# Kernel optimization log

Measured on AMD Instinct MI355X. Metric: run time of the kernel, lower is better.

## Reference

```python
import jax, jax.numpy as jnp
import numpy as np

NUM_REP = 3

def setup_inputs() -> dict:
    N, E, DIM, R2, L, B, NEG = 20000, 100000, 32, 100, 4, 4, 32
    ks = jax.random.split(jax.random.key(0), 12)
    # all negatives in a row share the same head (required by the model's assert)
    h = jax.random.randint(ks[0], (B, 1), 0, N)
    t = jax.random.randint(ks[1], (B, NEG), 0, N)
    batch = jnp.stack([jnp.broadcast_to(h, (B, NEG)), t], axis=-1)  # [B,NEG,2]
    edge_index = jax.random.randint(ks[2], (2, E), 0, N)
    edge_type = jax.random.randint(ks[3], (E,), 0, R2)
    edge_attr = 0.1 * jax.random.normal(ks[4], (E, DIM), jnp.float32)
    start_query = jax.random.normal(ks[5], (NUM_REP, DIM), jnp.float32)
    W_rel = jax.random.normal(ks[6], (L, DIM, R2 * DIM), jnp.float32) * (DIM ** -0.5)
    b_rel = jnp.zeros((L, R2 * DIM), jnp.float32)
    W_lin = jax.random.normal(ks[7], (L, 2 * DIM, DIM), jnp.float32) * ((2 * DIM) ** -0.5)
    b_lin = jnp.zeros((L, DIM), jnp.float32)
    W_mlp1 = jax.random.normal(ks[8], (DIM, DIM), jnp.float32) * (DIM ** -0.5)
    b_mlp1 = jnp.zeros((DIM,), jnp.float32)
    W_mlp2 = jax.random.normal(ks[9], (DIM, DIM), jnp.float32) * (DIM ** -0.5)
    b_mlp2 = jnp.zeros((DIM,), jnp.float32)
    return {"batch": batch, "edge_index": edge_index, "edge_type": edge_type,
            "edge_attr": edge_attr, "num_nodes": N, "start_query": start_query,
            "W_rel": W_rel, "b_rel": b_rel, "W_lin": W_lin, "b_lin": b_lin,
            "W_mlp1": W_mlp1, "b_mlp1": b_mlp1, "W_mlp2": W_mlp2, "b_mlp2": b_mlp2}

def reference(batch, edge_index, edge_type, edge_attr, num_nodes, start_query,
              W_rel, b_rel, W_lin, b_lin, W_mlp1, b_mlp1, W_mlp2, b_mlp2):
    B, num_neg, _ = batch.shape
    N = int(num_nodes)
    dim = start_query.shape[1]
    L = W_rel.shape[0]
    bs = NUM_REP * B
    batch_full = jnp.tile(batch, (NUM_REP, 1, 1))            # [bs, neg, 2]
    query_idx = jnp.repeat(jnp.arange(NUM_REP), B)           # [bs]
    h_index, t_index = batch_full[..., 0], batch_full[..., 1]
    # negative_sample_to_tail (no-op when heads are constant per row, as built)
    is_t_neg = jnp.all(h_index == h_index[:, :1], axis=-1, keepdims=True)
    h_index, t_index = (jnp.where(is_t_neg, h_index, t_index),
                        jnp.where(is_t_neg, t_index, h_index))
    h0 = h_index[:, 0]
    q = start_query[query_idx]                               # [bs, dim]
    rows = jnp.arange(bs)
    boundary = jnp.zeros((bs, N, dim), q.dtype).at[rows, h0].add(q)
    pb = jnp.zeros((bs, N), q.dtype).at[rows, h0].set(1.0)   # path boundary
    src, dst = edge_index[0], edge_index[1]
    x = boundary
    for l in range(L):
        # dependent per-query relation embeddings: [bs, 2R, dim]
        rel = (q @ W_rel[l] + b_rel[l]).reshape(bs, -1, dim)
        rel_e = rel[:, edge_type] + edge_attr[None]          # [bs, E, dim]
        msg = x[:, src] * rel_e                              # distmult message
        # sum aggregation; boundary acts as the self-loop message
        agg = jnp.zeros((bs, N, dim), x.dtype).at[:, dst].add(msg) + boundary
        x = jax.nn.relu(jnp.concatenate([x, agg], axis=-1) @ W_lin[l] + b_lin[l])
        # reachability propagation of the path boundary (scatter-max)
        pb = jnp.maximum(pb, jnp.zeros((bs, N), pb.dtype).at[:, dst].max(pb[:, src]))
    feat_t = x[rows[:, None], t_index]                       # [bs, neg, dim]
    feat = feat_t.reshape(NUM_REP, B, num_neg, dim).mean(0)  # mean over reps
    features = jax.nn.relu(feat @ W_mlp1 + b_mlp1) @ W_mlp2 + b_mlp2
    pb_t = pb[rows[:, None], t_index][..., None]             # [bs, neg, 1]
    path_boundary = pb_t.reshape(NUM_REP, B, num_neg, 1).max(0)
    return features, path_boundary
```

## Files before the change

### kernel.cpp

```cpp
#include <hip/hip_runtime.h>

#define N_NODES 20000
#define N_EDGES 100000
#define DIM 32
#define R2 100
#define NLAYERS 4
#define BATCH 4
#define NEG 32
#define NREP 3
#define BS (NREP * BATCH)
#define RELDIM (R2 * DIM)

#define NPB 4
#define TPN 96
#define LBLK (NPB * TPN)
#define GRID_LAYER (N_NODES / NPB)

#define XO_A 0
#define XO_B (XO_A + (size_t)N_NODES * BS * DIM)
#define PBO_A (XO_B + (size_t)N_NODES * BS * DIM)
#define PBO_B (PBO_A + (size_t)N_NODES * BS)
#define RELO (PBO_B + (size_t)N_NODES * BS)
#define QO (RELO + (size_t)NLAYERS * R2 * BS * DIM)
#define FLOAT_TOTAL (QO + (size_t)BS * DIM)

#define IO_H0 0
#define IO_TIDX (IO_H0 + BS)
#define IO_COUNTS (IO_TIDX + BS * NEG)
#define IO_OFF (IO_COUNTS + N_NODES)
#define IO_CURSOR (IO_OFF + N_NODES + 1)
#define IO_PERM (IO_CURSOR + N_NODES)
#define INT_TOTAL (IO_PERM + N_EDGES)

__global__ void k_init(const int* __restrict__ batch,
                       const float* __restrict__ start_query,
                       float* __restrict__ q, int* __restrict__ h0,
                       int* __restrict__ t_idx) {
    int r = threadIdx.x;
    if (r >= BS) return;
    int b = r % BATCH, rep = r / BATCH;
    int h00 = batch[(b * NEG + 0) * 2 + 0];
    bool is_t_neg = true;
    for (int j = 0; j < NEG; j++)
        if (batch[(b * NEG + j) * 2 + 0] != h00) { is_t_neg = false; break; }
    int hsel = is_t_neg ? 0 : 1;
    int h0v = batch[(b * NEG + 0) * 2 + hsel];
    h0[r] = h0v;
    for (int j = 0; j < NEG; j++)
        t_idx[r * NEG + j] = batch[(b * NEG + j) * 2 + (1 - hsel)];
    for (int d = 0; d < DIM; d++) q[r * DIM + d] = start_query[rep * DIM + d];
}

__global__ void k_count(const int* __restrict__ dst, int* __restrict__ counts) {
    int e = blockIdx.x * blockDim.x + threadIdx.x;
    if (e < N_EDGES) atomicAdd(&counts[dst[e]], 1);
}

__global__ void k_scan(const int* __restrict__ counts, int* __restrict__ off,
                       int* __restrict__ cursor) {
    __shared__ int sd[1024];
    int t = threadIdx.x;
    const int CH = (N_NODES + 1023) / 1024;
    int base = t * CH;
    int sum = 0;
    for (int i = 0; i < CH; i++) {
        int idx = base + i;
        if (idx < N_NODES) sum += counts[idx];
    }
    sd[t] = sum;
    __syncthreads();
    for (int o = 1; o < 1024; o <<= 1) {
        int v = (t >= o) ? sd[t - o] : 0;
        __syncthreads();
        sd[t] += v;
        __syncthreads();
    }
    int excl = sd[t] - sum;
    int run = excl;
    for (int i = 0; i < CH; i++) {
        int idx = base + i;
        if (idx < N_NODES) {
            off[idx] = run;
            cursor[idx] = run;
            run += counts[idx];
        }
    }
    if (t == 1023) off[N_NODES] = sd[1023];
}

__global__ void k_place(const int* __restrict__ dst, int* __restrict__ cursor,
                        int* __restrict__ perm) {
    int e = blockIdx.x * blockDim.x + threadIdx.x;
    if (e < N_EDGES) {
        int p = atomicAdd(&cursor[dst[e]], 1);
        perm[p] = e;
    }
}

__global__ void k_rel_all(const float* __restrict__ q, const float* __restrict__ W_rel,
                          const float* __restrict__ b_rel, float* __restrict__ rel) {
    int idx = blockIdx.x * blockDim.x + threadIdx.x;
    if (idx >= NLAYERS * R2 * BS * DIM) return;
    int d = idx & 31;
    int r = (idx >> 5) % BS;
    int et = (idx / (BS * DIM)) % R2;
    int l = idx / (R2 * BS * DIM);
    int c = et * DIM + d;
    const float* W = W_rel + (size_t)l * DIM * RELDIM;
    float acc = b_rel[l * RELDIM + c];
    #pragma unroll
    for (int k = 0; k < DIM; k++) acc += q[r * DIM + k] * W[(size_t)k * RELDIM + c];
    rel[idx] = acc;
}

template <bool L0>
__launch_bounds__(LBLK)
__global__ void k_layer(const float* __restrict__ x_old, const float* __restrict__ pb_old,
                        const float* __restrict__ rel_l, const float* __restrict__ edge_attr,
                        const int* __restrict__ src, const int* __restrict__ etype,
                        const int* __restrict__ off, const int* __restrict__ perm,
                        const int* __restrict__ h0, const float* __restrict__ q,
                        const float* __restrict__ W_lin_l, const float* __restrict__ b_lin_l,
                        float* __restrict__ x_new, float* __restrict__ pb_new) {
    __shared__ float sW[64 * DIM];
    __shared__ float sB[DIM];
    __shared__ float sIn[NPB * BS * 68];

    for (int i = threadIdx.x; i < 64 * DIM; i += LBLK) sW[i] = W_lin_l[i];
    if (threadIdx.x < DIM) sB[threadIdx.x] = b_lin_l[threadIdx.x];

    const int gi = threadIdx.x / TPN;
    const int t = threadIdx.x % TPN;
    const int r = t >> 3;
    const int l = t & 7;
    const int n = blockIdx.x * NPB + gi;

    const int h0r = h0[r];
    const float4 q4 = *(const float4*)(q + r * DIM + l * 4);

    float4 xr4, ag4 = make_float4(0.f, 0.f, 0.f, 0.f);
    float pbm;
    if (L0) {
        xr4 = (n == h0r) ? q4 : make_float4(0.f, 0.f, 0.f, 0.f);
        pbm = (n == h0r) ? 1.f : 0.f;
    } else {
        xr4 = *(const float4*)(x_old + ((size_t)n * BS + r) * DIM + l * 4);
        pbm = pb_old[n * BS + r];
    }

    const int s0 = off[n], s1 = off[n + 1];
    for (int k = s0; k < s1; k++) {
        int e = perm[k];
        int s = src[e];
        if (L0) {
            if (s == h0r) {
                int et = etype[e];
                float4 rl = *(const float4*)(rel_l + ((size_t)et * BS + r) * DIM + l * 4);
                float4 ea = *(const float4*)(edge_attr + (size_t)e * DIM + l * 4);
                ag4.x += q4.x * (rl.x + ea.x);
                ag4.y += q4.y * (rl.y + ea.y);
                ag4.z += q4.z * (rl.z + ea.z);
                ag4.w += q4.w * (rl.w + ea.w);
                pbm = 1.f;
            }
        } else {
            int et = etype[e];
            float4 xs = *(const float4*)(x_old + ((size_t)s * BS + r) * DIM + l * 4);
            float4 rl = *(const float4*)(rel_l + ((size_t)et * BS + r) * DIM + l * 4);
            float4 ea = *(const float4*)(edge_attr + (size_t)e * DIM + l * 4);
            ag4.x += xs.x * (rl.x + ea.x);
            ag4.y += xs.y * (rl.y + ea.y);
            ag4.z += xs.z * (rl.z + ea.z);
            ag4.w += xs.w * (rl.w + ea.w);
            pbm = fmaxf(pbm, pb_old[s * BS + r]);
        }
    }
    if (n == h0r) {
        ag4.x += q4.x; ag4.y += q4.y; ag4.z += q4.z; ag4.w += q4.w;
    }

    float* srow = sIn + (gi * BS + r) * 68;
    *(float4*)(srow + l * 4) = xr4;
    *(float4*)(srow + 32 + l * 4) = ag4;
    __syncthreads();

    float4 acc = *(const float4*)(sB + l * 4);
    #pragma unroll
    for (int k4 = 0; k4 < 16; k4++) {
        float4 v = *(const float4*)(srow + k4 * 4);
        const float* wb = sW + (k4 * 4) * DIM + l * 4;
        float4 w0 = *(const float4*)(wb);
        float4 w1 = *(const float4*)(wb + DIM);
        float4 w2 = *(const float4*)(wb + 2 * DIM);
        float4 w3 = *(const float4*)(wb + 3 * DIM);
        acc.x += v.x * w0.x + v.y * w1.x + v.z * w2.x + v.w * w3.x;
        acc.y += v.x * w0.y + v.y * w1.y + v.z * w2.y + v.w * w3.y;
        acc.z += v.x * w0.z + v.y * w1.z + v.z * w2.z + v.w * w3.z;
        acc.w += v.x * w0.w + v.y * w1.w + v.z * w2.w + v.w * w3.w;
    }
    acc.x = fmaxf(acc.x, 0.f);
    acc.y = fmaxf(acc.y, 0.f);
    acc.z = fmaxf(acc.z, 0.f);
    acc.w = fmaxf(acc.w, 0.f);
    *(float4*)(x_new + ((size_t)n * BS + r) * DIM + l * 4) = acc;
    if (l == 0) pb_new[n * BS + r] = pbm;
}

__launch_bounds__(1024)
__global__ void k_final(const float* __restrict__ x, const float* __restrict__ pb,
                        const int* __restrict__ t_idx,
                        const float* __restrict__ W1, const float* __restrict__ b1,
                        const float* __restrict__ W2, const float* __restrict__ b2,
                        float* __restrict__ out) {
    __shared__ float sW1[DIM * DIM];
    __shared__ float sW2[DIM * DIM];
    __shared__ float sfeat[BATCH * NEG * DIM];
    __shared__ float shid[BATCH * NEG * DIM];
    const int t = threadIdx.x;
    const int NPAIR = BATCH * NEG;

    for (int i = t; i < DIM * DIM; i += 1024) { sW1[i] = W1[i]; sW2[i] = W2[i]; }

    for (int i = t; i < NPAIR * DIM; i += 1024) {
        int pair = i >> 5;
        int d = i & 31;
        int b = pair >> 5;
        int tt = t_idx[pair];
        float s = 0.f;
        #pragma unroll
        for (int rep = 0; rep < NREP; rep++)
            s += x[((size_t)tt * BS + rep * BATCH + b) * DIM + d];
        sfeat[i] = s * (1.f / 3.f);
    }
    __syncthreads();

    for (int i = t; i < NPAIR * DIM; i += 1024) {
        int pair = i >> 5;
        int jj = i & 31;
        float a = b1[jj];
        #pragma unroll
        for (int k = 0; k < DIM; k++)
            a += sfeat[pair * DIM + k] * sW1[k * DIM + jj];
        shid[i] = fmaxf(a, 0.f);
    }
    __syncthreads();

    for (int i = t; i < NPAIR * DIM; i += 1024) {
        int pair = i >> 5;
        int jj = i & 31;
        float a = b2[jj];
        #pragma unroll
        for (int k = 0; k < DIM; k++)
            a += shid[pair * DIM + k] * sW2[k * DIM + jj];
        out[i] = a;
    }

    if (t < NPAIR) {
        int b = t >> 5;
        int tt = t_idx[t];
        float pm = 0.f;
        #pragma unroll
        for (int rep = 0; rep < NREP; rep++)
            pm = fmaxf(pm, pb[(size_t)tt * BS + rep * BATCH + b]);
        out[NPAIR * DIM + t] = pm;
    }
}

extern "C" void kernel_launch(void* const* d_in, const int* in_sizes, int n_in,
                              void* d_out, int out_size, void* d_ws, size_t ws_size,
                              hipStream_t stream) {
    const int* batch = (const int*)d_in[0];
    const int* edge_index = (const int*)d_in[1];
    const int* edge_type = (const int*)d_in[2];
    const float* edge_attr = (const float*)d_in[3];
    const float* start_query = (const float*)d_in[5];
    const float* W_rel = (const float*)d_in[6];
    const float* b_rel = (const float*)d_in[7];
    const float* W_lin = (const float*)d_in[8];
    const float* b_lin = (const float*)d_in[9];
    const float* W_mlp1 = (const float*)d_in[10];
    const float* b_mlp1 = (const float*)d_in[11];
    const float* W_mlp2 = (const float*)d_in[12];
    const float* b_mlp2 = (const float*)d_in[13];

    float* wf = (float*)d_ws;
    int* wi = (int*)(wf + FLOAT_TOTAL);
    size_t need = FLOAT_TOTAL * sizeof(float) + INT_TOTAL * sizeof(int);
    if (ws_size < need) return;

    float* x_a = wf + XO_A;
    float* x_b = wf + XO_B;
    float* pb_a = wf + PBO_A;
    float* pb_b = wf + PBO_B;
    float* rel = wf + RELO;
    float* q = wf + QO;
    int* h0 = wi + IO_H0;
    int* t_idx = wi + IO_TIDX;
    int* counts = wi + IO_COUNTS;
    int* off = wi + IO_OFF;
    int* cursor = wi + IO_CURSOR;
    int* perm = wi + IO_PERM;

    const int* src = edge_index;
    const int* dst = edge_index + N_EDGES;

    hipMemsetAsync(counts, 0, (size_t)N_NODES * sizeof(int), stream);

    k_init<<<1, 64, 0, stream>>>(batch, start_query, q, h0, t_idx);

    int eb = (N_EDGES + 255) / 256;
    k_count<<<eb, 256, 0, stream>>>(dst, counts);
    k_scan<<<1, 1024, 0, stream>>>(counts, off, cursor);
    k_place<<<eb, 256, 0, stream>>>(dst, cursor, perm);

    int relb = (NLAYERS * R2 * BS * DIM + 255) / 256;
    k_rel_all<<<relb, 256, 0, stream>>>(q, W_rel, b_rel, rel);

    k_layer<true><<<GRID_LAYER, LBLK, 0, stream>>>(
        x_a, pb_a, rel, edge_attr, src, edge_type, off, perm, h0, q,
        W_lin, b_lin, x_a, pb_a);

    float* x_cur = x_a;
    float* x_nxt = x_b;
    float* pb_cur = pb_a;
    float* pb_nxt = pb_b;
    for (int l = 1; l < NLAYERS; l++) {
        k_layer<false><<<GRID_LAYER, LBLK, 0, stream>>>(
            x_cur, pb_cur, rel + (size_t)l * R2 * BS * DIM, edge_attr, src, edge_type,
            off, perm, h0, q,
            W_lin + (size_t)l * 64 * DIM, b_lin + (size_t)l * DIM,
            x_nxt, pb_nxt);
        float* tx = x_cur; x_cur = x_nxt; x_nxt = tx;
        float* tp = pb_cur; pb_cur = pb_nxt; pb_nxt = tp;
    }

    k_final<<<1, 1024, 0, stream>>>(x_cur, pb_cur, t_idx, W_mlp1, b_mlp1, W_mlp2, b_mlp2,
                                    (float*)d_out);
}
```

Before: 376.3 us.

## Pack edge metadata, sort nodes by degree, and fast-path unreached nodes in layer 0

Edges are now stored in dst-sorted order as packed (src|etype<<20, edge id) pairs, so each layer's gather loop does one coalesced int2 load instead of the perm→src→etype chain. A degree histogram and an extra ordering kernel assign nodes to blocks in degree order, so the NPB nodes sharing a block have similar work. In layer 0, blocks whose nodes have no edge from any query head skip the weight load and matmul and write relu(bias) directly. This adds a histogram, an extra launch and a flag sync in exchange, and it assumes node ids fit in 20 bits and edge types fit in the remaining 12.

```diff
diff --git a/kernel.cpp b/kernel.cpp
--- a/kernel.cpp
+++ b/kernel.cpp
@@ -28,9 +28,12 @@
 #define IO_TIDX (IO_H0 + BS)
 #define IO_COUNTS (IO_TIDX + BS * NEG)
 #define IO_OFF (IO_COUNTS + N_NODES)
-#define IO_CURSOR (IO_OFF + N_NODES + 1)
-#define IO_PERM (IO_CURSOR + N_NODES)
-#define INT_TOTAL (IO_PERM + N_EDGES)
+#define IO_BCUR (IO_OFF + N_NODES + 1)
+#define IO_CURSOR (IO_BCUR + 256)
+#define IO_ORDER (IO_CURSOR + N_NODES)
+#define IO_PAD (IO_ORDER + N_NODES)
+#define IO_ES (((IO_PAD + 1) / 2) * 2)
+#define INT_TOTAL (IO_ES + 2 * N_EDGES)
 
 __global__ void k_init(const int* __restrict__ batch,
                        const float* __restrict__ start_query,
@@ -57,11 +60,13 @@
 }
 
 __global__ void k_scan(const int* __restrict__ counts, int* __restrict__ off,
-                       int* __restrict__ cursor) {
+                       int* __restrict__ cursor, int* __restrict__ bcursor) {
     __shared__ int sd[1024];
+    __shared__ int hist[256];
     int t = threadIdx.x;
     const int CH = (N_NODES + 1023) / 1024;
     int base = t * CH;
+    for (int i = t; i < 256; i += 1024) hist[i] = 0;
     int sum = 0;
     for (int i = 0; i < CH; i++) {
         int idx = base + i;
@@ -80,20 +85,38 @@
     for (int i = 0; i < CH; i++) {
         int idx = base + i;
         if (idx < N_NODES) {
+            int c = counts[idx];
             off[idx] = run;
             cursor[idx] = run;
-            run += counts[idx];
+            run += c;
+            atomicAdd(&hist[c < 255 ? c : 255], 1);
         }
     }
     if (t == 1023) off[N_NODES] = sd[1023];
-}
-
-__global__ void k_place(const int* __restrict__ dst, int* __restrict__ cursor,
-                        int* __restrict__ perm) {
+    __syncthreads();
+    if (t == 0) {
+        int acc = 0;
+        for (int b = 0; b < 256; b++) { bcursor[b] = acc; acc += hist[b]; }
+    }
+}
+
+__global__ void k_place(const int* __restrict__ src, const int* __restrict__ dst,
+                        const int* __restrict__ etype, int* __restrict__ cursor,
+                        int2* __restrict__ es) {
     int e = blockIdx.x * blockDim.x + threadIdx.x;
     if (e < N_EDGES) {
         int p = atomicAdd(&cursor[dst[e]], 1);
-        perm[p] = e;
+        es[p] = make_int2(src[e] | (etype[e] << 20), e);
+    }
+}
+
+__global__ void k_order(const int* __restrict__ counts, int* __restrict__ bcursor,
+                        int* __restrict__ node_order) {
+    int n = blockIdx.x * blockDim.x + threadIdx.x;
+    if (n < N_NODES) {
+        int deg = counts[n]; if (deg > 255) deg = 255;
+        int pos = atomicAdd(&bcursor[deg], 1);
+        node_order[pos] = n;
     }
 }
 
@@ -117,26 +140,48 @@
 __launch_bounds__(LBLK)
 __global__ void k_layer(const float* __restrict__ x_old, const float* __restrict__ pb_old,
                         const float* __restrict__ rel_l, const float* __restrict__ edge_attr,
-                        const int* __restrict__ src, const int* __restrict__ etype,
-                        const int* __restrict__ off, const int* __restrict__ perm,
+                        const int2* __restrict__ es, const int* __restrict__ off,
+                        const int* __restrict__ node_order,
                         const int* __restrict__ h0, const float* __restrict__ q,
                         const float* __restrict__ W_lin_l, const float* __restrict__ b_lin_l,
                         float* __restrict__ x_new, float* __restrict__ pb_new) {
     __shared__ float sW[64 * DIM];
     __shared__ float sB[DIM];
     __shared__ float sIn[NPB * BS * 68];
-
-    for (int i = threadIdx.x; i < 64 * DIM; i += LBLK) sW[i] = W_lin_l[i];
-    if (threadIdx.x < DIM) sB[threadIdx.x] = b_lin_l[threadIdx.x];
+    __shared__ int sFlag;
 
     const int gi = threadIdx.x / TPN;
     const int t = threadIdx.x % TPN;
     const int r = t >> 3;
     const int l = t & 7;
-    const int n = blockIdx.x * NPB + gi;
+    const int n = node_order[blockIdx.x * NPB + gi];
 
     const int h0r = h0[r];
     const float4 q4 = *(const float4*)(q + r * DIM + l * 4);
+    const int s0 = off[n], s1 = off[n + 1];
+
+    if (L0) {
+        if (threadIdx.x == 0) sFlag = 0;
+        bool spec = (n == h0r);
+        for (int k = s0; k < s1; k++) {
+            int2 p2 = es[k];
+            if ((p2.x & 0xFFFFF) == h0r) spec = true;
+        }
+        __syncthreads();
+        if (spec) sFlag = 1;
+        __syncthreads();
+        if (!sFlag) {
+            float4 b4 = *(const float4*)(b_lin_l + l * 4);
+            b4.x = fmaxf(b4.x, 0.f); b4.y = fmaxf(b4.y, 0.f);
+            b4.z = fmaxf(b4.z, 0.f); b4.w = fmaxf(b4.w, 0.f);
+            *(float4*)(x_new + ((size_t)n * BS + r) * DIM + l * 4) = b4;
+            if (l == 0) pb_new[n * BS + r] = 0.f;
+            return;
+        }
+    }
+
+    for (int i = threadIdx.x; i < 64 * DIM; i += LBLK) sW[i] = W_lin_l[i];
+    if (threadIdx.x < DIM) sB[threadIdx.x] = b_lin_l[threadIdx.x];
 
     float4 xr4, ag4 = make_float4(0.f, 0.f, 0.f, 0.f);
     float pbm;
@@ -148,13 +193,13 @@
         pbm = pb_old[n * BS + r];
     }
 
-    const int s0 = off[n], s1 = off[n + 1];
     for (int k = s0; k < s1; k++) {
-        int e = perm[k];
-        int s = src[e];
+        int2 p2 = es[k];
+        int s = p2.x & 0xFFFFF;
+        int et = ((unsigned)p2.x) >> 20;
+        int e = p2.y;
         if (L0) {
             if (s == h0r) {
-                int et = etype[e];
                 float4 rl = *(const float4*)(rel_l + ((size_t)et * BS + r) * DIM + l * 4);
                 float4 ea = *(const float4*)(edge_attr + (size_t)e * DIM + l * 4);
                 ag4.x += q4.x * (rl.x + ea.x);
@@ -164,7 +209,6 @@
                 pbm = 1.f;
             }
         } else {
-            int et = etype[e];
             float4 xs = *(const float4*)(x_old + ((size_t)s * BS + r) * DIM + l * 4);
             float4 rl = *(const float4*)(rel_l + ((size_t)et * BS + r) * DIM + l * 4);
             float4 ea = *(const float4*)(edge_attr + (size_t)e * DIM + l * 4);
@@ -298,8 +342,10 @@
     int* t_idx = wi + IO_TIDX;
     int* counts = wi + IO_COUNTS;
     int* off = wi + IO_OFF;
+    int* bcursor = wi + IO_BCUR;
     int* cursor = wi + IO_CURSOR;
-    int* perm = wi + IO_PERM;
+    int* node_order = wi + IO_ORDER;
+    int2* es = (int2*)(wi + IO_ES);
 
     const int* src = edge_index;
     const int* dst = edge_index + N_EDGES;
@@ -309,15 +355,17 @@
     k_init<<<1, 64, 0, stream>>>(batch, start_query, q, h0, t_idx);
 
     int eb = (N_EDGES + 255) / 256;
+    int nb = (N_NODES + 255) / 256;
     k_count<<<eb, 256, 0, stream>>>(dst, counts);
-    k_scan<<<1, 1024, 0, stream>>>(counts, off, cursor);
-    k_place<<<eb, 256, 0, stream>>>(dst, cursor, perm);
+    k_scan<<<1, 1024, 0, stream>>>(counts, off, cursor, bcursor);
+    k_place<<<eb, 256, 0, stream>>>(src, dst, edge_type, cursor, es);
+    k_order<<<nb, 256, 0, stream>>>(counts, bcursor, node_order);
 
     int relb = (NLAYERS * R2 * BS * DIM + 255) / 256;
     k_rel_all<<<relb, 256, 0, stream>>>(q, W_rel, b_rel, rel);
 
     k_layer<true><<<GRID_LAYER, LBLK, 0, stream>>>(
-        x_a, pb_a, rel, edge_attr, src, edge_type, off, perm, h0, q,
+        x_a, pb_a, rel, edge_attr, es, off, node_order, h0, q,
         W_lin, b_lin, x_a, pb_a);
 
     float* x_cur = x_a;
@@ -326,8 +374,8 @@
     float* pb_nxt = pb_b;
     for (int l = 1; l < NLAYERS; l++) {
         k_layer<false><<<GRID_LAYER, LBLK, 0, stream>>>(
-            x_cur, pb_cur, rel + (size_t)l * R2 * BS * DIM, edge_attr, src, edge_type,
-            off, perm, h0, q,
+            x_cur, pb_cur, rel + (size_t)l * R2 * BS * DIM, edge_attr, es, off,
+            node_order, h0, q,
             W_lin + (size_t)l * 64 * DIM, b_lin + (size_t)l * DIM,
             x_nxt, pb_nxt);
         float* tx = x_cur; x_cur = x_nxt; x_nxt = tx;
```

Result: slower. 393.4 us (+4.5%).
